# Performance work log

Measured on AMD Instinct MI355X. Metric: run time of the kernel, lower is better.

Reference implementation:

```python
import jax, jax.numpy as jnp
import numpy as np

NUM_HEADS = 16


def _apply_rope(x, freqs):
    # x: (H, L, C), freqs: (L, C//2); computed in fp32, cast back to x.dtype
    xf = x.astype(jnp.float32)
    x1, x2 = jnp.split(xf, 2, axis=-1)
    f = freqs.astype(jnp.float32)[None]  # (1, L, C//2)
    cos, sin = jnp.cos(f), jnp.sin(f)
    out = jnp.concatenate((x1 * cos - x2 * sin, x1 * sin + x2 * cos), axis=-1)
    return out.astype(x.dtype)


def setup_inputs() -> dict:
    key = jax.random.key(0)
    k0, k1, k2, k3 = jax.random.split(key, 4)
    S, D, H = 4096, 1280, NUM_HEADS
    hd = D // H
    hidden_states = jax.random.normal(k0, (S, D), dtype=jnp.float32)
    cu_seqlens = jnp.array([0, 1024, 2048, 3072, 4096], dtype=jnp.int32)
    rotary_pos_emb = jax.random.normal(k1, (S, hd // 2), dtype=jnp.float32)
    scale = 1.0 / np.sqrt(D)
    w_qkv = (jax.random.normal(k2, (D, 3 * D), dtype=jnp.float32) * scale)
    b_qkv = jnp.zeros((3 * D,), dtype=jnp.float32)
    w_proj = (jax.random.normal(k3, (D, D), dtype=jnp.float32) * scale)
    b_proj = jnp.zeros((D,), dtype=jnp.float32)
    return {
        "hidden_states": hidden_states,
        "cu_seqlens": cu_seqlens,
        "rotary_pos_emb": rotary_pos_emb,
        "w_qkv": w_qkv,
        "b_qkv": b_qkv,
        "w_proj": w_proj,
        "b_proj": b_proj,
    }


def reference(hidden_states, cu_seqlens, rotary_pos_emb, w_qkv, b_qkv, w_proj, b_proj):
    S, D = hidden_states.shape
    H = NUM_HEADS
    hd = D // H
    qkv = hidden_states @ w_qkv + b_qkv            # (S, 3D)
    qkv = qkv.reshape(S, 3, H, hd).transpose(1, 2, 0, 3)  # (3, H, S, hd)
    q, k, v = qkv[0], qkv[1], qkv[2]
    q = _apply_rope(q, rotary_pos_emb)
    k = _apply_rope(k, rotary_pos_emb)
    # block-diagonal (per-segment) attention, equivalent to the per-segment loop
    seg = jnp.searchsorted(cu_seqlens, jnp.arange(S), side="right") - 1  # (S,)
    mask = seg[:, None] == seg[None, :]            # (S, S)
    scores = jnp.einsum("hqd,hkd->hqk", q, k) / np.sqrt(hd)
    scores = jnp.where(mask[None], scores, -jnp.inf)
    attn = jax.nn.softmax(scores.astype(jnp.float32), axis=-1).astype(q.dtype)
    out = jnp.einsum("hqk,hkd->qhd", attn, v).reshape(S, D)
    return out @ w_proj + b_proj
```

## Files before the change

### kernel.cpp

```cpp
#include <hip/hip_runtime.h>
#include <hip/hip_bf16.h>
#include <cstdint>

typedef __bf16 bf16x8 __attribute__((ext_vector_type(8)));
typedef __bf16 bf16x4 __attribute__((ext_vector_type(4)));
typedef short short4_ __attribute__((ext_vector_type(4)));
typedef float f32x4 __attribute__((ext_vector_type(4)));

#define SLEN 4096
#define DMODEL 1280
#define NHEADS 16
#define HD 80
#define HDP 96
#define VTILE_ELEMS 3328
#define VTILE_LDS 3584

#define GLD_LDS16(g, l)                                                        \
  __builtin_amdgcn_global_load_lds(                                            \
      (const __attribute__((address_space(1))) void*)(g),                      \
      (__attribute__((address_space(3))) void*)(l), 16, 0, 0)

#define WAIT_VMCNT(n) __builtin_amdgcn_s_waitcnt((n & 0xF) | 0x70 | 0xF00 | ((n >> 4) << 14))

#define FENCE asm volatile("" ::: "memory")
#define BARRIER do { FENCE; __builtin_amdgcn_s_barrier(); FENCE; } while (0)

__device__ __forceinline__ void transpose_body(const float* __restrict__ in,
                                               __bf16* __restrict__ out,
                                               int K, int N, int bx, int by, int t) {
  __shared__ float tile[32][33];
  int n0 = bx * 32, k0 = by * 32;
  int x = t & 31, y = t >> 5;
  for (int i = 0; i < 32; i += 8)
    tile[y + i][x] = in[(size_t)(k0 + y + i) * N + n0 + x];
  __syncthreads();
  for (int i = 0; i < 32; i += 8)
    out[(size_t)(n0 + y + i) * K + k0 + x] = (__bf16)tile[x][y + i];
}

__global__ __launch_bounds__(256) void prep(const float* __restrict__ hidden,
                                            __bf16* __restrict__ hid_b,
                                            const float* __restrict__ w_qkv,
                                            __bf16* __restrict__ wqkvT,
                                            const float* __restrict__ w_proj,
                                            __bf16* __restrict__ wprojT) {
  int bid = blockIdx.x, t = threadIdx.x;
  if (bid < 5120) {
    int i = bid * 256 + t;
    float4 v = ((const float4*)hidden)[i];
    bf16x4 o = { (__bf16)v.x, (__bf16)v.y, (__bf16)v.z, (__bf16)v.w };
    ((bf16x4*)hid_b)[i] = o;
  } else if (bid < 9920) {
    int b = bid - 5120;
    transpose_body(w_qkv, wqkvT, 1280, 3840, b % 120, b / 120, t);
  } else {
    int b = bid - 9920;
    transpose_body(w_proj, wprojT, 1280, 1280, b % 40, b / 40, t);
  }
}

template <int I0, int J0>
__device__ __forceinline__ void mfma16(f32x4 (&acc)[8][4], bf16x8 (&af)[4][2],
                                       bf16x8 (&bfr)[4][2]) {
  __builtin_amdgcn_s_setprio(1);
#pragma unroll
  for (int kk = 0; kk < 2; ++kk)
#pragma unroll
    for (int i = 0; i < 4; ++i)
#pragma unroll
      for (int j = 0; j < 2; ++j)
        acc[I0 + i][J0 + j] = __builtin_amdgcn_mfma_f32_16x16x32_bf16(
            bfr[J0 + j][kk], af[i][kk], acc[I0 + i][J0 + j], 0, 0, 0);
  __builtin_amdgcn_s_setprio(0);
}

__global__ __launch_bounds__(512, 2) void gemm256(const __bf16* __restrict__ A,
                                                  const __bf16* __restrict__ Bt,
                                                  const float* __restrict__ bias,
                                                  __bf16* __restrict__ C,
                                                  int M, int N, int K) {
  __shared__ __attribute__((aligned(1024))) __bf16 As[2][256 * 64];
  __shared__ __attribute__((aligned(1024))) __bf16 Bs[2][256 * 64];

  const int t = threadIdx.x;
  const int lane = t & 63, wave = t >> 6;
  const int quad = lane >> 4, l15 = lane & 15;
  const int wm = wave >> 2, wn = wave & 3;

  const int mb = M >> 8;
  const int cpx = gridDim.x >> 3;
  const int wg = (blockIdx.x & 7) * cpx + (blockIdx.x >> 3);
  const int bm = (wg % mb) * 256, bn = (wg / mb) * 256;

  const __bf16* Ab = A + (size_t)bm * K;
  const __bf16* Bb = Bt + (size_t)bn * K;

  auto stage = [&](const __bf16* g, __bf16* l, int row0, int kt) {
    GLD_LDS16(g + (size_t)(row0 + (lane >> 3)) * K + kt * 64 +
                  (((lane & 7) ^ ((lane >> 3) & 7)) << 3),
              l + row0 * 64);
  };
  auto lda = [&](bf16x8 (&dst)[4][2], const __bf16* Al, int I0) {
#pragma unroll
    for (int i = 0; i < 4; ++i)
#pragma unroll
      for (int kk = 0; kk < 2; ++kk) {
        int row = wm * 128 + (I0 + i) * 16 + l15;
        int c = (kk * 64 + quad * 16) ^ ((l15 & 7) << 4);
        dst[i][kk] = *(const bf16x8*)&Al[row * 64 + (c >> 1)];
      }
  };
  auto ldb = [&](bf16x8 (&dst)[2][2], const __bf16* Bl, int J0) {
#pragma unroll
    for (int j = 0; j < 2; ++j)
#pragma unroll
      for (int kk = 0; kk < 2; ++kk) {
        int row = wn * 64 + (J0 + j) * 16 + l15;
        int c = (kk * 64 + quad * 16) ^ ((l15 & 7) << 4);
        dst[j][kk] = *(const bf16x8*)&Bl[row * 64 + (c >> 1)];
      }
  };

  const int aw = wave * 8;
  const int be0 = (wave >> 2) * 64 + (wave & 3) * 8;
  const int niter = K >> 6;

  stage(Ab, As[0], aw, 0);        stage(Ab, As[0], 128 + aw, 0);
  stage(Bb, Bs[0], be0, 0);       stage(Bb, Bs[0], be0 + 128, 0);
  stage(Ab, As[0], 64 + aw, 0);   stage(Ab, As[0], 192 + aw, 0);
  stage(Bb, Bs[0], be0 + 32, 0);  stage(Bb, Bs[0], be0 + 160, 0);
  stage(Ab, As[1], aw, 1);        stage(Ab, As[1], 128 + aw, 1);
  stage(Bb, Bs[1], be0, 1);       stage(Bb, Bs[1], be0 + 128, 1);
  WAIT_VMCNT(4);
  BARRIER;

  f32x4 acc[8][4] = {};
  bf16x8 af[4][2], bfr[4][2];

  for (int it = 0; it < niter; ++it) {
    const int cur = it & 1;
    const __bf16* Ac = As[cur];
    const __bf16* Bc = Bs[cur];
    __bf16* An = As[cur ^ 1];
    __bf16* Bn = Bs[cur ^ 1];
    const bool p1 = it + 1 < niter, p2 = it + 2 < niter;

    lda(af, Ac, 0);
    ldb(reinterpret_cast<bf16x8(&)[2][2]>(bfr[0]), Bc, 0);
    if (p1) { stage(Ab, An, 64 + aw, it + 1); stage(Ab, An, 192 + aw, it + 1); }
    BARRIER;
    mfma16<0, 0>(acc, af, bfr);
    BARRIER;

    ldb(reinterpret_cast<bf16x8(&)[2][2]>(bfr[2]), Bc, 2);
    if (p1) { stage(Bb, Bn, be0 + 32, it + 1); stage(Bb, Bn, be0 + 160, it + 1); }
    BARRIER;
    mfma16<0, 2>(acc, af, bfr);
    BARRIER;

    lda(af, Ac, 4);
    if (p2) { stage(Ab, (__bf16*)Ac, aw, it + 2); stage(Ab, (__bf16*)Ac, 128 + aw, it + 2); }
    BARRIER;
    mfma16<4, 0>(acc, af, bfr);
    BARRIER;

    if (p2) { stage(Bb, (__bf16*)Bc, be0, it + 2); stage(Bb, (__bf16*)Bc, be0 + 128, it + 2); }
    BARRIER;
    mfma16<4, 2>(acc, af, bfr);
    WAIT_VMCNT(4);
    BARRIER;
  }

  float4 bv[4];
#pragma unroll
  for (int j = 0; j < 4; ++j)
    bv[j] = *(const float4*)&bias[bn + wn * 64 + j * 16 + quad * 4];
#pragma unroll
  for (int i = 0; i < 8; ++i) {
    size_t row = (size_t)(bm + wm * 128 + i * 16 + l15);
#pragma unroll
    for (int j = 0; j < 4; ++j) {
      int col = bn + wn * 64 + j * 16 + quad * 4;
      const float* bp = (const float*)&bv[j];
      bf16x4 ov;
#pragma unroll
      for (int r = 0; r < 4; ++r) ov[r] = (__bf16)(acc[i][j][r] + bp[r]);
      *(bf16x4*)&C[row * N + col] = ov;
    }
  }
}

template <int WMW>
__global__ __launch_bounds__(WMW * 2 * 64) void gemm_bt(const __bf16* __restrict__ A,
                                                        const __bf16* __restrict__ Bt,
                                                        const float* __restrict__ bias,
                                                        void* __restrict__ C,
                                                        int M, int N, int K, int store_bf16) {
  constexpr int BM = WMW * 64;
  constexpr int NW = WMW * 2;
  constexpr int BI = 8 / NW;
  constexpr int PW = 2 + BI;
  constexpr int ASZ = BM * 32, BSZ = 128 * 32;

  __shared__ __attribute__((aligned(16))) __bf16 As[3][ASZ];
  __shared__ __attribute__((aligned(16))) __bf16 Bs[3][BSZ];

  const int t = threadIdx.x;
  const int lane = t & 63, wave = t >> 6;
  const int quad = lane >> 4, l15 = lane & 15;
  const int wm = (wave & (WMW - 1)) * 64, wn = (wave / WMW) * 64;
  const int bm = blockIdx.x * BM, bn = blockIdx.y * 128;

  const int rs = lane >> 2, cs = (lane & 3) * 8;
  const __bf16* AgQ[2];
  const __bf16* BgQ[BI];
  int aLds[2], bLds[BI];
#pragma unroll
  for (int q = 0; q < 2; ++q) {
    int row = (wave * 2 + q) * 16;
    AgQ[q] = A + (size_t)(bm + row + rs) * K + cs;
    aLds[q] = row * 32;
  }
#pragma unroll
  for (int q = 0; q < BI; ++q) {
    int row = (wave * BI + q) * 16;
    BgQ[q] = Bt + (size_t)(bn + row + rs) * K + cs;
    bLds[q] = row * 32;
  }

  f32x4 acc[4][4] = {};
  const int niter = K >> 5;

#pragma unroll
  for (int s = 0; s < 2; ++s) {
#pragma unroll
    for (int q = 0; q < 2; ++q) GLD_LDS16(AgQ[q] + s * 32, &As[s][aLds[q]]);
#pragma unroll
    for (int q = 0; q < BI; ++q) GLD_LDS16(BgQ[q] + s * 32, &Bs[s][bLds[q]]);
  }

  int cmp = 0, stg = 2;
  for (int it = 0; it < niter; ++it) {
    const int kk = (it + 2 < niter ? it + 2 : niter - 1) * 32;
#pragma unroll
    for (int q = 0; q < 2; ++q) GLD_LDS16(AgQ[q] + kk, &As[stg][aLds[q]]);
#pragma unroll
    for (int q = 0; q < BI; ++q) GLD_LDS16(BgQ[q] + kk, &Bs[stg][bLds[q]]);
    asm volatile("" ::: "memory");
    WAIT_VMCNT(2 * PW);
    __builtin_amdgcn_s_barrier();
    asm volatile("" ::: "memory");

    bf16x8 af[4], bfr[4];
#pragma unroll
    for (int i = 0; i < 4; ++i)
      af[i] = *(const bf16x8*)&As[cmp][(wm + i * 16 + l15) * 32 + quad * 8];
#pragma unroll
    for (int j = 0; j < 4; ++j)
      bfr[j] = *(const bf16x8*)&Bs[cmp][(wn + j * 16 + l15) * 32 + quad * 8];
#pragma unroll
    for (int i = 0; i < 4; ++i)
#pragma unroll
      for (int j = 0; j < 4; ++j)
        acc[i][j] = __builtin_amdgcn_mfma_f32_16x16x32_bf16(bfr[j], af[i], acc[i][j], 0, 0, 0);

    asm volatile("" ::: "memory");
    __builtin_amdgcn_s_barrier();
    asm volatile("" ::: "memory");
    cmp = (cmp == 2) ? 0 : cmp + 1;
    stg = (stg == 2) ? 0 : stg + 1;
  }

  float4 bv[4];
#pragma unroll
  for (int j = 0; j < 4; ++j)
    bv[j] = *(const float4*)&bias[bn + wn + j * 16 + quad * 4];
#pragma unroll
  for (int i = 0; i < 4; ++i) {
    size_t row = (size_t)(bm + wm + i * 16 + l15);
#pragma unroll
    for (int j = 0; j < 4; ++j) {
      int col = bn + wn + j * 16 + quad * 4;
      const float* bp = (const float*)&bv[j];
      if (store_bf16) {
        bf16x4 ov;
#pragma unroll
        for (int r = 0; r < 4; ++r) ov[r] = (__bf16)(acc[i][j][r] + bp[r]);
        *(bf16x4*)&((__bf16*)C)[row * N + col] = ov;
      } else {
        float4 fv;
        fv.x = acc[i][j][0] + bp[0];
        fv.y = acc[i][j][1] + bp[1];
        fv.z = acc[i][j][2] + bp[2];
        fv.w = acc[i][j][3] + bp[3];
        *(float4*)&((float*)C)[row * N + col] = fv;
      }
    }
  }
}

__global__ __launch_bounds__(256) void rope_pack(const __bf16* __restrict__ qkv,
                                                 const float* __restrict__ freqs,
                                                 __bf16* __restrict__ qp,
                                                 __bf16* __restrict__ kp,
                                                 __bf16* __restrict__ vt) {
  const float QSCALE = 0.11180339887498949f * 1.44269504088896340f;
  int h = blockIdx.y;
  int s0 = blockIdx.x * 64;
  int t = threadIdx.x;
  int sp = t >> 2, l4 = t & 3;
  int s = s0 + sp;
  const __bf16* row = qkv + (size_t)s * 3840 + h * 80;
  __bf16* qo = qp + (size_t)(h * SLEN + s) * HDP;
  __bf16* ko = kp + (size_t)(h * SLEN + s) * HDP;

  __shared__ float vtile[64][81];

  for (int c = l4; c < 10; c += 4) {
    int base = (c < 5) ? c * 8 : (c - 5) * 8;
    bf16x8 xa = *(const bf16x8*)(row + base);
    bf16x8 xb = *(const bf16x8*)(row + base + 40);
    bf16x8 ya = *(const bf16x8*)(row + 1280 + base);
    bf16x8 yb = *(const bf16x8*)(row + 1280 + base + 40);
    float4 f0 = *(const float4*)(freqs + s * 40 + base);
    float4 f1 = *(const float4*)(freqs + s * 40 + base + 4);
    float fr[8] = {f0.x, f0.y, f0.z, f0.w, f1.x, f1.y, f1.z, f1.w};
    bf16x8 qv, kv;
#pragma unroll
    for (int e = 0; e < 8; ++e) {
      float cs = __builtin_cosf(fr[e]), sn = __builtin_sinf(fr[e]);
      float x1 = (float)xa[e], x2 = (float)xb[e];
      float y1 = (float)ya[e], y2 = (float)yb[e];
      float qvv, kvv;
      if (c < 5) { qvv = x1 * cs - x2 * sn; kvv = y1 * cs - y2 * sn; }
      else       { qvv = x1 * sn + x2 * cs; kvv = y1 * sn + y2 * cs; }
      qv[e] = (__bf16)(qvv * QSCALE);
      kv[e] = (__bf16)kvv;
    }
    *(bf16x8*)(qo + c * 8) = qv;
    *(bf16x8*)(ko + c * 8) = kv;
  }
  {
    bf16x8 z = {};
    if (l4 == 0) *(bf16x8*)(qo + 80) = z;
    if (l4 == 1) *(bf16x8*)(qo + 88) = z;
    if (l4 == 2) *(bf16x8*)(ko + 80) = z;
    if (l4 == 3) *(bf16x8*)(ko + 88) = z;
  }

  for (int c = l4; c < 10; c += 4) {
    bf16x8 v = *(const bf16x8*)(row + 2560 + c * 8);
#pragma unroll
    for (int e = 0; e < 8; ++e)
      vtile[sp][c * 8 + e] = (float)v[e];
  }
  __syncthreads();

  for (int idx = t; idx < 640; idx += 256) {
    int c2 = idx >= 320;
    int rem = idx - (c2 ? 320 : 0);
    int d = rem >> 2, kc = rem & 3;
    __bf16* tb = vt + (size_t)(h * (SLEN / 32) + (s0 >> 5) + c2) * VTILE_ELEMS;
    bf16x8 ov;
#pragma unroll
    for (int r = 0; r < 4; ++r) {
      ov[r]     = (__bf16)vtile[c2 * 32 + kc * 4 + r][d];
      ov[r + 4] = (__bf16)vtile[c2 * 32 + 16 + kc * 4 + r][d];
    }
    *(bf16x8*)(tb + d * 40 + kc * 8) = ov;
  }
}

__global__ __launch_bounds__(256) void flash_attn(const __bf16* __restrict__ qp,
                                                  const __bf16* __restrict__ kp,
                                                  const __bf16* __restrict__ vt,
                                                  const int* __restrict__ cu, int nseg,
                                                  __bf16* __restrict__ out) {
  const float MEXP = 16.0f;
  int h = blockIdx.y;
  int q0 = blockIdx.x * 128;
  int seg = 0;
  for (int i = 1; i < nseg; ++i)
    if (cu[i] <= q0) seg = i;
  int kstart = cu[seg], kend = cu[seg + 1];

  int t = threadIdx.x;
  int lane = t & 63, wave = t >> 6;
  int quad = lane >> 4, l15 = lane & 15;

  __shared__ __attribute__((aligned(16))) __bf16 Ks[2][64 * HDP];
  __shared__ __attribute__((aligned(16))) __bf16 Vs[2][2 * VTILE_LDS];

  bf16x8 qf[2][3];
#pragma unroll
  for (int qs = 0; qs < 2; ++qs) {
    const __bf16* qptr = qp + (size_t)(h * SLEN + q0 + wave * 32 + qs * 16 + l15) * HDP + quad * 8;
    qf[qs][0] = *(const bf16x8*)(qptr);
    qf[qs][1] = *(const bf16x8*)(qptr + 32);
    qf[qs][2] = *(const bf16x8*)(qptr + 64);
  }

  f32x4 o[2][5] = {};
  float l_p[2] = {0.f, 0.f};

  const __bf16* gK = kp + (size_t)(h * SLEN + kstart) * HDP + lane * 8;
  const __bf16* gV = vt + (size_t)(h * (SLEN / 32) + (kstart >> 5)) * VTILE_ELEMS + lane * 8;

  const int niter = (kend - kstart) >> 6;

  auto stage = [&](int kn, int buf) {
    const __bf16* ksrc = gK + (size_t)kn * (64 * HDP);
    const __bf16* vsrc = gV + (size_t)kn * (2 * VTILE_ELEMS);
#pragma unroll
    for (int i0 = 0; i0 < 7; ++i0) {
      int i = wave * 7 + i0;
      int ii = i < 26 ? i : 25;
      if (ii < 12)
        GLD_LDS16(ksrc + ii * 512, &Ks[buf][ii * 512]);
      else if (ii < 19)
        GLD_LDS16(vsrc + (ii - 12) * 512, &Vs[buf][(ii - 12) * 512]);
      else
        GLD_LDS16(vsrc + VTILE_ELEMS + (ii - 19) * 512, &Vs[buf][VTILE_LDS + (ii - 19) * 512]);
    }
  };

  stage(0, 0);

  for (int it = 0; it < niter; ++it) {
    const int cur = it & 1, nxt = cur ^ 1;
    const int kn = (it + 1 < niter) ? it + 1 : niter - 1;
    stage(kn, nxt);
    asm volatile("" ::: "memory");
    WAIT_VMCNT(7);
    __builtin_amdgcn_s_barrier();
    asm volatile("" ::: "memory");

    f32x4 sc[2][4];
#pragma unroll
    for (int nt = 0; nt < 4; ++nt) {
      sc[0][nt] = f32x4{-MEXP, -MEXP, -MEXP, -MEXP};
      sc[1][nt] = sc[0][nt];
#pragma unroll
      for (int c = 0; c < 3; ++c) {
        bf16x8 kf = *(const bf16x8*)&Ks[cur][(nt * 16 + l15) * HDP + quad * 8 + c * 32];
        sc[0][nt] = __builtin_amdgcn_mfma_f32_16x16x32_bf16(kf, qf[0][c], sc[0][nt], 0, 0, 0);
        sc[1][nt] = __builtin_amdgcn_mfma_f32_16x16x32_bf16(kf, qf[1][c], sc[1][nt], 0, 0, 0);
      }
    }

    bf16x4 pf[2][4];
#pragma unroll
    for (int qs = 0; qs < 2; ++qs)
#pragma unroll
      for (int nt = 0; nt < 4; ++nt)
#pragma unroll
        for (int r = 0; r < 4; ++r) {
          float p = __builtin_amdgcn_exp2f(sc[qs][nt][r]);
          l_p[qs] += p;
          pf[qs][nt][r] = (__bf16)p;
        }

#pragma unroll
    for (int g = 0; g < 2; ++g) {
#pragma unroll
      for (int dt = 0; dt < 5; ++dt) {
        bf16x8 vv = *(const bf16x8*)&Vs[cur][g * VTILE_LDS + (dt * 16 + l15) * 40 + quad * 8];
        bf16x4 vlo = __builtin_shufflevector(vv, vv, 0, 1, 2, 3);
        bf16x4 vhi = __builtin_shufflevector(vv, vv, 4, 5, 6, 7);
#pragma unroll
        for (int qs = 0; qs < 2; ++qs) {
          o[qs][dt] = __builtin_amdgcn_mfma_f32_16x16x16bf16_1k(
              *(short4_*)&vlo, *(short4_*)&pf[qs][g * 2], o[qs][dt], 0, 0, 0);
          o[qs][dt] = __builtin_amdgcn_mfma_f32_16x16x16bf16_1k(
              *(short4_*)&vhi, *(short4_*)&pf[qs][g * 2 + 1], o[qs][dt], 0, 0, 0);
        }
      }
    }

    asm volatile("" ::: "memory");
    __builtin_amdgcn_s_barrier();
    asm volatile("" ::: "memory");
  }

#pragma unroll
  for (int qs = 0; qs < 2; ++qs) {
    float l = l_p[qs];
    l += __shfl_xor(l, 16);
    l += __shfl_xor(l, 32);
    float rinv = 1.0f / l;
    int qrow = q0 + wave * 32 + qs * 16 + l15;
#pragma unroll
    for (int dt = 0; dt < 5; ++dt) {
      bf16x4 ov;
#pragma unroll
      for (int r = 0; r < 4; ++r)
        ov[r] = (__bf16)(o[qs][dt][r] * rinv);
      *(bf16x4*)&out[(size_t)qrow * DMODEL + h * 80 + dt * 16 + quad * 4] = ov;
    }
  }
}

extern "C" void kernel_launch(void* const* d_in, const int* in_sizes, int n_in,
                              void* d_out, int out_size, void* d_ws, size_t ws_size,
                              hipStream_t stream) {
  const float* hidden = (const float*)d_in[0];
  const int* cu       = (const int*)d_in[1];
  const float* freqs  = (const float*)d_in[2];
  const float* w_qkv  = (const float*)d_in[3];
  const float* b_qkv  = (const float*)d_in[4];
  const float* w_proj = (const float*)d_in[5];
  const float* b_proj = (const float*)d_in[6];
  float* out = (float*)d_out;

  char* ws = (char*)d_ws;
  size_t off = 0;
  auto alloc = [&](size_t bytes) {
    char* p = ws + off;
    off += (bytes + 255) & ~(size_t)255;
    return p;
  };
  __bf16* hid_b  = (__bf16*)alloc((size_t)SLEN * DMODEL * 2);
  __bf16* wqkvT  = (__bf16*)alloc((size_t)3840 * 1280 * 2);
  __bf16* wprojT = (__bf16*)alloc((size_t)1280 * 1280 * 2);
  __bf16* qkvb   = (__bf16*)alloc((size_t)SLEN * 3840 * 2);
  __bf16* qp     = (__bf16*)alloc((size_t)NHEADS * SLEN * HDP * 2);
  __bf16* kp     = (__bf16*)alloc((size_t)NHEADS * SLEN * HDP * 2 + 1024);
  __bf16* vt     = (__bf16*)alloc((size_t)NHEADS * (SLEN / 32) * VTILE_ELEMS * 2 + 1024);
  __bf16* attn   = hid_b;

  prep<<<11520, 256, 0, stream>>>(hidden, hid_b, w_qkv, wqkvT, w_proj, wprojT);
  gemm256<<<dim3((SLEN / 256) * (3840 / 256)), 512, 0, stream>>>(hid_b, wqkvT, b_qkv, qkvb,
                                                                 SLEN, 3840, 1280);
  rope_pack<<<dim3(SLEN / 64, NHEADS), 256, 0, stream>>>(qkvb, freqs, qp, kp, vt);
  int nseg = in_sizes[1] - 1;
  flash_attn<<<dim3(SLEN / 128, NHEADS), 256, 0, stream>>>(qp, kp, vt, cu, nseg, attn);
  gemm_bt<2><<<dim3(SLEN / 128, DMODEL / 128), 256, 0, stream>>>(attn, wprojT, b_proj, out,
                                                                 SLEN, DMODEL, 1280, 0);
}
```

Before: 237.0 us.

## Restructure GEMM LDS layout into k-halves with simplified double buffering

Splits each 64-wide K tile in shared memory into two 32-wide halves with a new XOR swizzle. The main loop now runs four phases per tile, each loading fragments for one k-half and one row half and issuing 16 MFMAs. The old scheme prefetched two tiles ahead with split staging; the new one uses plain double buffering that prefetches the next tile by halves. This simplifies fragment registers and changes the LDS bank-conflict pattern, but the shallower prefetch may expose more global-load latency.

```diff
diff --git a/kernel.cpp b/kernel.cpp
--- a/kernel.cpp
+++ b/kernel.cpp
@@ -59,18 +59,16 @@
   }
 }
 
-template <int I0, int J0>
-__device__ __forceinline__ void mfma16(f32x4 (&acc)[8][4], bf16x8 (&af)[4][2],
-                                       bf16x8 (&bfr)[4][2]) {
+template <int RH>
+__device__ __forceinline__ void mm16(f32x4 (&acc)[8][4], bf16x8 (&af)[4],
+                                     bf16x8 (&bf)[4]) {
   __builtin_amdgcn_s_setprio(1);
 #pragma unroll
-  for (int kk = 0; kk < 2; ++kk)
-#pragma unroll
-    for (int i = 0; i < 4; ++i)
-#pragma unroll
-      for (int j = 0; j < 2; ++j)
-        acc[I0 + i][J0 + j] = __builtin_amdgcn_mfma_f32_16x16x32_bf16(
-            bfr[J0 + j][kk], af[i][kk], acc[I0 + i][J0 + j], 0, 0, 0);
+  for (int i = 0; i < 4; ++i)
+#pragma unroll
+    for (int j = 0; j < 4; ++j)
+      acc[RH * 4 + i][j] = __builtin_amdgcn_mfma_f32_16x16x32_bf16(
+          bf[j], af[i], acc[RH * 4 + i][j], 0, 0, 0);
   __builtin_amdgcn_s_setprio(0);
 }
 
@@ -79,8 +77,8 @@
                                                   const float* __restrict__ bias,
                                                   __bf16* __restrict__ C,
                                                   int M, int N, int K) {
-  __shared__ __attribute__((aligned(1024))) __bf16 As[2][256 * 64];
-  __shared__ __attribute__((aligned(1024))) __bf16 Bs[2][256 * 64];
+  __shared__ __attribute__((aligned(1024))) __bf16 As[2][2][256 * 32];
+  __shared__ __attribute__((aligned(1024))) __bf16 Bs[2][2][256 * 32];
 
   const int t = threadIdx.x;
   const int lane = t & 63, wave = t >> 6;
@@ -95,79 +93,83 @@
   const __bf16* Ab = A + (size_t)bm * K;
   const __bf16* Bb = Bt + (size_t)bn * K;
 
-  auto stage = [&](const __bf16* g, __bf16* l, int row0, int kt) {
-    GLD_LDS16(g + (size_t)(row0 + (lane >> 3)) * K + kt * 64 +
-                  (((lane & 7) ^ ((lane >> 3) & 7)) << 3),
-              l + row0 * 64);
+  const int srow = (lane >> 2);
+  const int scol = ((lane & 3) ^ (srow & 3)) << 3;
+  auto stA = [&](int buf, int kh, int kt) {
+#pragma unroll
+    for (int j = 0; j < 2; ++j) {
+      int R = wave * 32 + j * 16;
+      GLD_LDS16(Ab + (size_t)(R + srow) * K + kt * 64 + kh * 32 + scol,
+                &As[buf][kh][R * 32]);
+    }
   };
-  auto lda = [&](bf16x8 (&dst)[4][2], const __bf16* Al, int I0) {
-#pragma unroll
-    for (int i = 0; i < 4; ++i)
-#pragma unroll
-      for (int kk = 0; kk < 2; ++kk) {
-        int row = wm * 128 + (I0 + i) * 16 + l15;
-        int c = (kk * 64 + quad * 16) ^ ((l15 & 7) << 4);
-        dst[i][kk] = *(const bf16x8*)&Al[row * 64 + (c >> 1)];
-      }
+  auto stB = [&](int buf, int kh, int kt) {
+#pragma unroll
+    for (int j = 0; j < 2; ++j) {
+      int R = wave * 32 + j * 16;
+      GLD_LDS16(Bb + (size_t)(R + srow) * K + kt * 64 + kh * 32 + scol,
+                &Bs[buf][kh][R * 32]);
+    }
   };
-  auto ldb = [&](bf16x8 (&dst)[2][2], const __bf16* Bl, int J0) {
-#pragma unroll
-    for (int j = 0; j < 2; ++j)
-#pragma unroll
-      for (int kk = 0; kk < 2; ++kk) {
-        int row = wn * 64 + (J0 + j) * 16 + l15;
-        int c = (kk * 64 + quad * 16) ^ ((l15 & 7) << 4);
-        dst[j][kk] = *(const bf16x8*)&Bl[row * 64 + (c >> 1)];
-      }
+
+  const int rslot = (lane & 3);
+  auto ldA = [&](bf16x8 (&dst)[4], const __bf16* base, int rh) {
+#pragma unroll
+    for (int i = 0; i < 4; ++i) {
+      int row = wm * 128 + rh * 64 + i * 16 + l15;
+      dst[i] = *(const bf16x8*)&base[row * 32 + ((quad ^ rslot) << 3)];
+    }
   };
-
-  const int aw = wave * 8;
-  const int be0 = (wave >> 2) * 64 + (wave & 3) * 8;
+  auto ldB = [&](bf16x8 (&dst)[4], const __bf16* base) {
+#pragma unroll
+    for (int j = 0; j < 4; ++j) {
+      int row = wn * 64 + j * 16 + l15;
+      dst[j] = *(const bf16x8*)&base[row * 32 + ((quad ^ rslot) << 3)];
+    }
+  };
+
   const int niter = K >> 6;
 
-  stage(Ab, As[0], aw, 0);        stage(Ab, As[0], 128 + aw, 0);
-  stage(Bb, Bs[0], be0, 0);       stage(Bb, Bs[0], be0 + 128, 0);
-  stage(Ab, As[0], 64 + aw, 0);   stage(Ab, As[0], 192 + aw, 0);
-  stage(Bb, Bs[0], be0 + 32, 0);  stage(Bb, Bs[0], be0 + 160, 0);
-  stage(Ab, As[1], aw, 1);        stage(Ab, As[1], 128 + aw, 1);
-  stage(Bb, Bs[1], be0, 1);       stage(Bb, Bs[1], be0 + 128, 1);
+  stA(0, 0, 0); stB(0, 0, 0);
+  stA(0, 1, 0); stB(0, 1, 0);
   WAIT_VMCNT(4);
   BARRIER;
 
   f32x4 acc[8][4] = {};
-  bf16x8 af[4][2], bfr[4][2];
-
-  for (int it = 0; it < niter; ++it) {
-    const int cur = it & 1;
-    const __bf16* Ac = As[cur];
-    const __bf16* Bc = Bs[cur];
-    __bf16* An = As[cur ^ 1];
-    __bf16* Bn = Bs[cur ^ 1];
-    const bool p1 = it + 1 < niter, p2 = it + 2 < niter;
-
-    lda(af, Ac, 0);
-    ldb(reinterpret_cast<bf16x8(&)[2][2]>(bfr[0]), Bc, 0);
-    if (p1) { stage(Ab, An, 64 + aw, it + 1); stage(Ab, An, 192 + aw, it + 1); }
-    BARRIER;
-    mfma16<0, 0>(acc, af, bfr);
-    BARRIER;
-
-    ldb(reinterpret_cast<bf16x8(&)[2][2]>(bfr[2]), Bc, 2);
-    if (p1) { stage(Bb, Bn, be0 + 32, it + 1); stage(Bb, Bn, be0 + 160, it + 1); }
-    BARRIER;
-    mfma16<0, 2>(acc, af, bfr);
-    BARRIER;
-
-    lda(af, Ac, 4);
-    if (p2) { stage(Ab, (__bf16*)Ac, aw, it + 2); stage(Ab, (__bf16*)Ac, 128 + aw, it + 2); }
-    BARRIER;
-    mfma16<4, 0>(acc, af, bfr);
-    BARRIER;
-
-    if (p2) { stage(Bb, (__bf16*)Bc, be0, it + 2); stage(Bb, (__bf16*)Bc, be0 + 128, it + 2); }
-    BARRIER;
-    mfma16<4, 2>(acc, af, bfr);
-    WAIT_VMCNT(4);
+  bf16x8 af[4], bf_[4];
+
+  for (int T = 0; T < niter; ++T) {
+    const int buf = T & 1, nb = buf ^ 1;
+    const __bf16* A0k = &As[buf][0][0];
+    const __bf16* A1k = &As[buf][1][0];
+    const __bf16* B0k = &Bs[buf][0][0];
+    const __bf16* B1k = &Bs[buf][1][0];
+    const bool p1 = T + 1 < niter;
+
+    ldA(af, A0k, 0); ldB(bf_, B0k);
+    if (p1) stA(nb, 0, T + 1);
+    BARRIER;
+    mm16<0>(acc, af, bf_);
+    BARRIER;
+
+    ldA(af, A0k, 1);
+    if (p1) stB(nb, 0, T + 1);
+    BARRIER;
+    mm16<1>(acc, af, bf_);
+    if (p1) { WAIT_VMCNT(4); } else { WAIT_VMCNT(0); }
+    BARRIER;
+
+    ldA(af, A1k, 0); ldB(bf_, B1k);
+    if (p1) stA(nb, 1, T + 1);
+    BARRIER;
+    mm16<0>(acc, af, bf_);
+    BARRIER;
+
+    ldA(af, A1k, 1);
+    if (p1) stB(nb, 1, T + 1);
+    BARRIER;
+    mm16<1>(acc, af, bf_);
+    if (p1) { WAIT_VMCNT(4); }
     BARRIER;
   }
 
```

After: 243.4 us. +2.7%, slower.
